# Kernel optimization log

Measured on AMD Instinct MI355X. Metric: run time of the kernel, lower is better.

Reference implementation:

```python
import jax, jax.numpy as jnp
import numpy as np

R = 0.2                 # radius (init kwarg r)
MAX_NEIGHBORS = 32      # init kwarg max_num_neighbors
N = 16384
N_BATCH = 8


def setup_inputs() -> dict:
    key = jax.random.key(0)
    k1, k2, k3, k4 = jax.random.split(key, 4)
    node_coord_src = jax.random.uniform(k1, (N, 3), dtype=jnp.float32)
    node_coord_dst = jax.random.uniform(k2, (N, 3), dtype=jnp.float32)
    batch_src = jnp.sort(jax.random.randint(k3, (N,), 0, N_BATCH, dtype=jnp.int64))
    batch_dst = jnp.sort(jax.random.randint(k4, (N,), 0, N_BATCH, dtype=jnp.int64))
    return {
        "node_coord_src": node_coord_src,
        "batch_src": batch_src,
        "node_coord_dst": node_coord_dst,
        "batch_dst": batch_dst,
    }


def reference(node_coord_src, batch_src, node_coord_dst, batch_dst):
    """Batch-aware radius graph: for each dst point, up to MAX_NEIGHBORS src
    points within radius R and in the same batch (deterministically the
    lowest-index ones). Returns fixed-shape padded (edge_src, edge_dst),
    padded with -1 where fewer than MAX_NEIGHBORS neighbors exist."""
    n_src = node_coord_src.shape[0]
    n_dst = node_coord_dst.shape[0]

    # squared pairwise distances [n_dst, n_src] without [N,N,3] intermediate
    s2 = jnp.sum(node_coord_src * node_coord_src, axis=-1)          # [n_src]
    d2 = jnp.sum(node_coord_dst * node_coord_dst, axis=-1)          # [n_dst]
    cross = jnp.einsum("nd,md->nm", node_coord_dst, node_coord_src)  # [n_dst,n_src]
    dist2 = d2[:, None] + s2[None, :] - 2.0 * cross

    valid = (dist2 <= R * R) & (batch_dst[:, None] == batch_src[None, :])

    # pick first MAX_NEIGHBORS valid src indices per dst: encode src index,
    # invalid -> n_src (sentinel), take K smallest via top_k of negation
    src_idx = jnp.arange(n_src, dtype=jnp.int32)
    keyed = jnp.where(valid, src_idx[None, :], n_src)               # [n_dst,n_src]
    neg_sel, _ = jax.lax.top_k(-keyed, MAX_NEIGHBORS)
    sel = -neg_sel                                                  # [n_dst,K]
    found = sel < n_src

    edge_src = jnp.where(found, sel, -1)
    edge_dst = jnp.where(found, jnp.arange(n_dst, dtype=jnp.int32)[:, None], -1)
    return edge_src.reshape(-1), edge_dst.reshape(-1)
```

## Files before the change

### kernel.cpp

```cpp
#include <hip/hip_runtime.h>

#define K 32

__global__ __launch_bounds__(256) void RadiusConnect_kernel(
    const float* __restrict__ src_xyz, const int* __restrict__ batch_src,
    const float* __restrict__ dst_xyz, const int* __restrict__ batch_dst,
    int n_src, int n_dst, int* __restrict__ out)
{
    const int wave = (blockIdx.x * blockDim.x + threadIdx.x) >> 6;
    const int lane = threadIdx.x & 63;
    if (wave >= n_dst) return;
    const int d = wave;

    const float xd = dst_xyz[3 * d + 0];
    const float yd = dst_xyz[3 * d + 1];
    const float zd = dst_xyz[3 * d + 2];
    const float d2 = __fadd_rn(__fadd_rn(__fmul_rn(xd, xd), __fmul_rn(yd, yd)),
                               __fmul_rn(zd, zd));
    const int b = batch_dst[d];

    int lo = 0, hi = n_src;
    while (lo < hi) {
        int mid = (lo + hi) >> 1;
        if (batch_src[mid] < b) lo = mid + 1; else hi = mid;
    }
    const int start = lo;
    hi = n_src;
    while (lo < hi) {
        int mid = (lo + hi) >> 1;
        if (batch_src[mid] < b + 1) lo = mid + 1; else hi = mid;
    }
    const int end = lo;

    const float rr = __fmul_rn(0.2f, 0.2f);
    int* __restrict__ out_src = out;
    int* __restrict__ out_dst = out + (size_t)n_dst * K;
    const long long base = (long long)d * K;

    int count = 0;
    for (int j0 = start; j0 < end && count < K; j0 += 64) {
        const int j = j0 + lane;
        bool valid = false;
        if (j < end) {
            const float xs = src_xyz[3 * j + 0];
            const float ys = src_xyz[3 * j + 1];
            const float zs = src_xyz[3 * j + 2];
            const float s2 = __fadd_rn(
                __fadd_rn(__fmul_rn(xs, xs), __fmul_rn(ys, ys)),
                __fmul_rn(zs, zs));
            const float cross = __fadd_rn(
                __fadd_rn(__fmul_rn(xd, xs), __fmul_rn(yd, ys)),
                __fmul_rn(zd, zs));
            const float dist2 = __fsub_rn(__fadd_rn(d2, s2),
                                          __fmul_rn(2.0f, cross));
            valid = (dist2 <= rr);
        }
        const unsigned long long mask = __ballot(valid);
        const int pre = __popcll(mask & ((1ull << lane) - 1ull));
        const int rank = count + pre;
        if (valid && rank < K) {
            out_src[base + rank] = j;
            out_dst[base + rank] = d;
        }
        count += __popcll(mask);
    }

    if (count < K && lane >= count && lane < K) {
        out_src[base + lane] = -1;
        out_dst[base + lane] = -1;
    }
}

extern "C" void kernel_launch(void* const* d_in, const int* in_sizes, int n_in,
                              void* d_out, int out_size, void* d_ws, size_t ws_size,
                              hipStream_t stream) {
    const float* src_xyz   = (const float*)d_in[0];
    const int*   batch_src = (const int*)d_in[1];
    const float* dst_xyz   = (const float*)d_in[2];
    const int*   batch_dst = (const int*)d_in[3];
    int* out = (int*)d_out;

    const int n_src = in_sizes[0] / 3;
    const int n_dst = in_sizes[2] / 3;

    const int threads = 256;
    const int blocks = (n_dst * 64 + threads - 1) / threads;
    RadiusConnect_kernel<<<blocks, threads, 0, stream>>>(
        src_xyz, batch_src, dst_xyz, batch_dst, n_src, n_dst, out);
}
```

Baseline: 99.80 us.

## Precompute batch bounds in a tiny kernel and unroll the source scan by four

A small pre-kernel binary-searches the sorted batch_src once per batch id and writes the segment boundaries to workspace, so each destination wave no longer runs two binary searches over global memory. The main loop now loads four 64-wide chunks of source points per iteration before computing distances and ballots, which adds memory-level parallelism. The cost is one extra kernel launch, possible overscan past the 32-neighbor cutoff within a 256-wide chunk, and a hardcoded assumption of 8 batches.

```diff
diff --git a/kernel.cpp b/kernel.cpp
--- a/kernel.cpp
+++ b/kernel.cpp
@@ -1,11 +1,25 @@
 #include <hip/hip_runtime.h>
 
 #define K 32
+#define NB 8
+
+__global__ void bounds_kernel(const int* __restrict__ batch_src, int n_src,
+                              int* __restrict__ bounds) {
+    const int b = threadIdx.x;
+    if (b > NB) return;
+    int lo = 0, hi = n_src;
+    while (lo < hi) {
+        int mid = (lo + hi) >> 1;
+        if (batch_src[mid] < b) lo = mid + 1; else hi = mid;
+    }
+    bounds[b] = lo;
+}
 
 __global__ __launch_bounds__(256) void RadiusConnect_kernel(
-    const float* __restrict__ src_xyz, const int* __restrict__ batch_src,
+    const float* __restrict__ src_xyz,
     const float* __restrict__ dst_xyz, const int* __restrict__ batch_dst,
-    int n_src, int n_dst, int* __restrict__ out)
+    const int* __restrict__ bounds,
+    int n_dst, int* __restrict__ out)
 {
     const int wave = (blockIdx.x * blockDim.x + threadIdx.x) >> 6;
     const int lane = threadIdx.x & 63;
@@ -18,51 +32,51 @@
     const float d2 = __fadd_rn(__fadd_rn(__fmul_rn(xd, xd), __fmul_rn(yd, yd)),
                                __fmul_rn(zd, zd));
     const int b = batch_dst[d];
-
-    int lo = 0, hi = n_src;
-    while (lo < hi) {
-        int mid = (lo + hi) >> 1;
-        if (batch_src[mid] < b) lo = mid + 1; else hi = mid;
-    }
-    const int start = lo;
-    hi = n_src;
-    while (lo < hi) {
-        int mid = (lo + hi) >> 1;
-        if (batch_src[mid] < b + 1) lo = mid + 1; else hi = mid;
-    }
-    const int end = lo;
+    const int start = bounds[b];
+    const int end   = bounds[b + 1];
 
     const float rr = __fmul_rn(0.2f, 0.2f);
     int* __restrict__ out_src = out;
     int* __restrict__ out_dst = out + (size_t)n_dst * K;
     const long long base = (long long)d * K;
+    const unsigned long long lt_mask = (1ull << lane) - 1ull;
 
     int count = 0;
-    for (int j0 = start; j0 < end && count < K; j0 += 64) {
-        const int j = j0 + lane;
-        bool valid = false;
-        if (j < end) {
-            const float xs = src_xyz[3 * j + 0];
-            const float ys = src_xyz[3 * j + 1];
-            const float zs = src_xyz[3 * j + 2];
+    for (int j0 = start; j0 < end && count < K; j0 += 256) {
+        float xs[4], ys[4], zs[4];
+        int jj[4];
+#pragma unroll
+        for (int g = 0; g < 4; ++g) {
+            int j = j0 + g * 64 + lane;
+            jj[g] = j;
+            int jl = j < end ? j : end - 1;
+            xs[g] = src_xyz[3 * jl + 0];
+            ys[g] = src_xyz[3 * jl + 1];
+            zs[g] = src_xyz[3 * jl + 2];
+        }
+        bool valid[4];
+#pragma unroll
+        for (int g = 0; g < 4; ++g) {
             const float s2 = __fadd_rn(
-                __fadd_rn(__fmul_rn(xs, xs), __fmul_rn(ys, ys)),
-                __fmul_rn(zs, zs));
+                __fadd_rn(__fmul_rn(xs[g], xs[g]), __fmul_rn(ys[g], ys[g])),
+                __fmul_rn(zs[g], zs[g]));
             const float cross = __fadd_rn(
-                __fadd_rn(__fmul_rn(xd, xs), __fmul_rn(yd, ys)),
-                __fmul_rn(zd, zs));
+                __fadd_rn(__fmul_rn(xd, xs[g]), __fmul_rn(yd, ys[g])),
+                __fmul_rn(zd, zs[g]));
             const float dist2 = __fsub_rn(__fadd_rn(d2, s2),
                                           __fmul_rn(2.0f, cross));
-            valid = (dist2 <= rr);
+            valid[g] = (jj[g] < end) && (dist2 <= rr);
         }
-        const unsigned long long mask = __ballot(valid);
-        const int pre = __popcll(mask & ((1ull << lane) - 1ull));
-        const int rank = count + pre;
-        if (valid && rank < K) {
-            out_src[base + rank] = j;
-            out_dst[base + rank] = d;
+#pragma unroll
+        for (int g = 0; g < 4; ++g) {
+            const unsigned long long mask = __ballot(valid[g]);
+            const int rank = count + __popcll(mask & lt_mask);
+            if (valid[g] && rank < K) {
+                out_src[base + rank] = jj[g];
+                out_dst[base + rank] = d;
+            }
+            count += __popcll(mask);
         }
-        count += __popcll(mask);
     }
 
     if (count < K && lane >= count && lane < K) {
@@ -78,13 +92,16 @@
     const int*   batch_src = (const int*)d_in[1];
     const float* dst_xyz   = (const float*)d_in[2];
     const int*   batch_dst = (const int*)d_in[3];
-    int* out = (int*)d_out;
+    int* out    = (int*)d_out;
+    int* bounds = (int*)d_ws;
 
     const int n_src = in_sizes[0] / 3;
     const int n_dst = in_sizes[2] / 3;
 
+    bounds_kernel<<<1, 16, 0, stream>>>(batch_src, n_src, bounds);
+
     const int threads = 256;
     const int blocks = (n_dst * 64 + threads - 1) / threads;
     RadiusConnect_kernel<<<blocks, threads, 0, stream>>>(
-        src_xyz, batch_src, dst_xyz, batch_dst, n_src, n_dst, out);
+        src_xyz, dst_xyz, batch_dst, bounds, n_dst, out);
 }
```

Result: faster. 87.09 us (-12.7%).

## Split radius search into per-lane dst scan over src chunks plus merge pass

Applied to the files above, without the earlier changes.

Work is regrouped so that each lane owns one destination point and each of 16 waves per 64-destination group scans one slice of the source range. Source coordinates are read at uniform addresses across the wave, and the ballot/popcount compaction is replaced by simple per-lane counting. Partial neighbor lists and counts go to a workspace, and a separate merge kernel concatenates them in index order to reproduce the lowest-index selection. Per-batch bounds are now computed once in a tiny kernel instead of by every wave. In exchange, the early exit after 32 hits is lost, so every source in the batch range is evaluated, and there are three launches plus a large workspace round trip.

```diff
diff --git a/kernel.cpp b/kernel.cpp
--- a/kernel.cpp
+++ b/kernel.cpp
@@ -1,74 +1,107 @@
 #include <hip/hip_runtime.h>
 
 #define K 32
+#define NB 8
+#define S 16
 
-__global__ __launch_bounds__(256) void RadiusConnect_kernel(
-    const float* __restrict__ src_xyz, const int* __restrict__ batch_src,
-    const float* __restrict__ dst_xyz, const int* __restrict__ batch_dst,
-    int n_src, int n_dst, int* __restrict__ out)
-{
-    const int wave = (blockIdx.x * blockDim.x + threadIdx.x) >> 6;
-    const int lane = threadIdx.x & 63;
-    if (wave >= n_dst) return;
-    const int d = wave;
+#define CNT_OFF  4096
+#define SUB_OFF  (4096 + (1 << 20))
 
-    const float xd = dst_xyz[3 * d + 0];
-    const float yd = dst_xyz[3 * d + 1];
-    const float zd = dst_xyz[3 * d + 2];
-    const float d2 = __fadd_rn(__fadd_rn(__fmul_rn(xd, xd), __fmul_rn(yd, yd)),
-                               __fmul_rn(zd, zd));
-    const int b = batch_dst[d];
-
+__global__ void bounds_kernel(const int* __restrict__ batch_src, int n_src,
+                              int* __restrict__ bounds) {
+    const int b = threadIdx.x;
+    if (b > NB) return;
     int lo = 0, hi = n_src;
     while (lo < hi) {
         int mid = (lo + hi) >> 1;
         if (batch_src[mid] < b) lo = mid + 1; else hi = mid;
     }
-    const int start = lo;
-    hi = n_src;
-    while (lo < hi) {
-        int mid = (lo + hi) >> 1;
-        if (batch_src[mid] < b + 1) lo = mid + 1; else hi = mid;
-    }
-    const int end = lo;
+    bounds[b] = lo;
+}
 
-    const float rr = __fmul_rn(0.2f, 0.2f);
-    int* __restrict__ out_src = out;
-    int* __restrict__ out_dst = out + (size_t)n_dst * K;
-    const long long base = (long long)d * K;
+__global__ __launch_bounds__(256) void scan_kernel(
+    const float* __restrict__ src_xyz,
+    const float* __restrict__ dst_xyz, const int* __restrict__ batch_dst,
+    const int* __restrict__ bounds, int n_dst,
+    int* __restrict__ cnt, int* __restrict__ sub)
+{
+    const int tid  = blockIdx.x * blockDim.x + threadIdx.x;
+    const int wave = tid >> 6, lane = tid & 63;
+    const int g = wave / S, s = wave % S;
+    const int d  = g * 64 + lane;
+    const int dc = d < n_dst ? d : n_dst - 1;
+    const bool live = (d < n_dst);
+
+    const float xd = dst_xyz[3 * dc + 0];
+    const float yd = dst_xyz[3 * dc + 1];
+    const float zd = dst_xyz[3 * dc + 2];
+    const float d2 = __fadd_rn(__fadd_rn(__fmul_rn(xd, xd), __fmul_rn(yd, yd)),
+                               __fmul_rn(zd, zd));
+    const int b = batch_dst[dc];
+    const int my_lo = bounds[b];
+    const int my_hi = bounds[b + 1];
+
+    const int lo_w = __shfl(my_lo, 0);
+    const int hi_w = __shfl(my_hi, 63);
+    const int L    = (hi_w - lo_w + S - 1) / S;
+    const int c_lo = lo_w + s * L;
+    const int c_hi = min(c_lo + L, hi_w);
 
     int count = 0;
-    for (int j0 = start; j0 < end && count < K; j0 += 64) {
-        const int j = j0 + lane;
-        bool valid = false;
-        if (j < end) {
-            const float xs = src_xyz[3 * j + 0];
-            const float ys = src_xyz[3 * j + 1];
-            const float zs = src_xyz[3 * j + 2];
-            const float s2 = __fadd_rn(
-                __fadd_rn(__fmul_rn(xs, xs), __fmul_rn(ys, ys)),
-                __fmul_rn(zs, zs));
-            const float cross = __fadd_rn(
-                __fadd_rn(__fmul_rn(xd, xs), __fmul_rn(yd, ys)),
-                __fmul_rn(zd, zs));
-            const float dist2 = __fsub_rn(__fadd_rn(d2, s2),
-                                          __fmul_rn(2.0f, cross));
-            valid = (dist2 <= rr);
+    const long long base = ((long long)d * S + s) * K;
+
+#pragma unroll 4
+    for (int j = c_lo; j < c_hi; ++j) {
+        const float xs = src_xyz[3 * j + 0];
+        const float ys = src_xyz[3 * j + 1];
+        const float zs = src_xyz[3 * j + 2];
+        const float s2 = __fadd_rn(
+            __fadd_rn(__fmul_rn(xs, xs), __fmul_rn(ys, ys)),
+            __fmul_rn(zs, zs));
+        const float cross = __fadd_rn(
+            __fadd_rn(__fmul_rn(xd, xs), __fmul_rn(yd, ys)),
+            __fmul_rn(zd, zs));
+        const float dist2 = __fsub_rn(__fadd_rn(d2, s2),
+                                      __fmul_rn(2.0f, cross));
+        const bool valid = live && (dist2 <= 0.04f) &&
+                           (j >= my_lo) && (j < my_hi);
+        if (valid && count < K) {
+            sub[base + count] = j;
+            ++count;
         }
-        const unsigned long long mask = __ballot(valid);
-        const int pre = __popcll(mask & ((1ull << lane) - 1ull));
-        const int rank = count + pre;
-        if (valid && rank < K) {
-            out_src[base + rank] = j;
-            out_dst[base + rank] = d;
-        }
-        count += __popcll(mask);
     }
+    if (live) cnt[d * S + s] = count;
+}
 
-    if (count < K && lane >= count && lane < K) {
-        out_src[base + lane] = -1;
-        out_dst[base + lane] = -1;
+__global__ __launch_bounds__(256) void merge_kernel(
+    const int* __restrict__ cnt, const int* __restrict__ sub,
+    int n_dst, int* __restrict__ out)
+{
+    const int tid  = blockIdx.x * blockDim.x + threadIdx.x;
+    const int wave = tid >> 6, lane = tid & 63;
+    const int d = wave * 2 + (lane >> 5);
+    const int k = lane & 31;
+    if (d >= n_dst) return;
+
+    const int4* cp = (const int4*)(cnt + (size_t)d * S);
+    int cs[S];
+#pragma unroll
+    for (int q = 0; q < S / 4; ++q) {
+        const int4 a = cp[q];
+        cs[4 * q + 0] = a.x; cs[4 * q + 1] = a.y;
+        cs[4 * q + 2] = a.z; cs[4 * q + 3] = a.w;
     }
+    int pref = 0, sel_s = -1, sel_off = 0;
+#pragma unroll
+    for (int q = 0; q < S; ++q) {
+        const int off = k - pref;
+        if (off >= 0 && off < cs[q]) { sel_s = q; sel_off = off; }
+        pref += cs[q];
+    }
+    int val = -1;
+    if (sel_s >= 0) val = sub[((size_t)d * S + sel_s) * K + sel_off];
+    out[(size_t)d * K + k] = val;
+    out[(size_t)n_dst * K + (size_t)d * K + k] = (val >= 0) ? d : -1;
 }
 
 extern "C" void kernel_launch(void* const* d_in, const int* in_sizes, int n_in,
@@ -78,13 +111,22 @@
     const int*   batch_src = (const int*)d_in[1];
     const float* dst_xyz   = (const float*)d_in[2];
     const int*   batch_dst = (const int*)d_in[3];
-    int* out = (int*)d_out;
+    int* out    = (int*)d_out;
+    int* bounds = (int*)d_ws;
+    int* cnt    = (int*)((char*)d_ws + CNT_OFF);
+    int* sub    = (int*)((char*)d_ws + SUB_OFF);
 
     const int n_src = in_sizes[0] / 3;
     const int n_dst = in_sizes[2] / 3;
 
-    const int threads = 256;
-    const int blocks = (n_dst * 64 + threads - 1) / threads;
-    RadiusConnect_kernel<<<blocks, threads, 0, stream>>>(
-        src_xyz, batch_src, dst_xyz, batch_dst, n_src, n_dst, out);
+    bounds_kernel<<<1, 16, 0, stream>>>(batch_src, n_src, bounds);
+
+    const int G = (n_dst + 63) / 64;
+    const int waves1 = G * S;
+    scan_kernel<<<(waves1 * 64 + 255) / 256, 256, 0, stream>>>(
+        src_xyz, dst_xyz, batch_dst, bounds, n_dst, cnt, sub);
+
+    const int waves2 = (n_dst + 1) / 2;
+    merge_kernel<<<(waves2 * 64 + 255) / 256, 256, 0, stream>>>(
+        cnt, sub, n_dst, out);
 }
```

Result: slower. 150.2 us (+50.5%).
